# Optimization experiments

Measured on AMD Instinct MI355X. Metric: run time of the kernel, lower is better.

Reference implementation:

```python
import jax, jax.numpy as jnp
import numpy as np

VOCAB, EMBED, HIDDEN = 32000, 256, 1024
B, T = 64, 256


def setup_inputs() -> dict:
    key = jax.random.key(0)
    ks = jax.random.split(key, 8)
    s = 0.05
    return {
        "x": jax.random.randint(ks[0], (B, T), 0, VOCAB),
        "embed_table": jax.random.normal(ks[1], (VOCAB, EMBED), jnp.float32) * s,
        "W_ih": jax.random.normal(ks[2], (4 * HIDDEN, EMBED), jnp.float32) * s,
        "W_hh": jax.random.normal(ks[3], (4 * HIDDEN, HIDDEN), jnp.float32) * s,
        "b_ih": jax.random.normal(ks[4], (4 * HIDDEN,), jnp.float32) * s,
        "b_hh": jax.random.normal(ks[5], (4 * HIDDEN,), jnp.float32) * s,
        "fc_W": jax.random.normal(ks[6], (VOCAB, HIDDEN), jnp.float32) * s,
        "fc_b": jax.random.normal(ks[7], (VOCAB,), jnp.float32) * s,
    }


def _lstm_last_hidden(emb, W_ih, W_hh, b_ih, b_hh):
    # emb: [B, T, E]. PyTorch gate order: i, f, g, o.
    H = W_hh.shape[1]
    # Precompute input-side gate projections for all steps: [T, B, 4H]
    x_gates = jnp.einsum('bte,ge->tbg', emb, W_ih) + (b_ih + b_hh)

    def step(carry, xg):
        h, c = carry
        z = xg + h @ W_hh.T  # [B, 4H]
        i = jax.nn.sigmoid(z[:, 0 * H:1 * H])
        f = jax.nn.sigmoid(z[:, 1 * H:2 * H])
        g = jnp.tanh(z[:, 2 * H:3 * H])
        o = jax.nn.sigmoid(z[:, 3 * H:4 * H])
        c = f * c + i * g
        h = o * jnp.tanh(c)
        return (h, c), None

    bsz = emb.shape[0]
    h0 = jnp.zeros((bsz, H), emb.dtype)
    (h, _), _ = jax.lax.scan(step, (h0, h0), x_gates)
    return h  # last hidden state [B, H]


def reference(x, embed_table, W_ih, W_hh, b_ih, b_hh, fc_W, fc_b):
    emb = embed_table[x]  # [B, T, E]
    h_last = _lstm_last_hidden(emb, W_ih, W_hh, b_ih, b_hh)
    return h_last @ fc_W.T + fc_b  # [B, VOCAB]
```

## Files before the change

### kernel.cpp

```cpp
#include <hip/hip_runtime.h>
#include <hip/hip_bf16.h>

#define VOCAB  32000
#define EMBED  256
#define HIDDEN 1024
#define G4     4096
#define BATCH  64
#define SEQ    256

__global__ __launch_bounds__(256) void lstm_xgates(
    const int* __restrict__ x,
    const float* __restrict__ emb,
    const float* __restrict__ W_ih,
    const float* __restrict__ b_ih,
    const float* __restrict__ b_hh,
    float* __restrict__ xgT)
{
    const int t   = blockIdx.y;
    const int n0  = blockIdx.x * 64;
    const int tid = threadIdx.x;
    const int ty  = tid >> 4;
    const int tx  = tid & 15;

    __shared__ float As[64][36];
    __shared__ float Bs[64][36];
    __shared__ int   ridx[64];

    if (tid < 64) ridx[tid] = x[tid * SEQ + t];
    __syncthreads();

    float acc[4][4];
#pragma unroll
    for (int i = 0; i < 4; ++i)
#pragma unroll
        for (int j = 0; j < 4; ++j) acc[i][j] = 0.f;

    const int lr = tid >> 2;
    const int lc = (tid & 3) * 8;
    const float* abase = W_ih + (long)(n0 + lr) * EMBED + lc;
    const float* bbase = emb + (long)ridx[lr] * EMBED + lc;

    for (int k0 = 0; k0 < EMBED; k0 += 32) {
        *(float4*)&As[lr][lc]     = *(const float4*)(abase + k0);
        *(float4*)&As[lr][lc + 4] = *(const float4*)(abase + k0 + 4);
        *(float4*)&Bs[lr][lc]     = *(const float4*)(bbase + k0);
        *(float4*)&Bs[lr][lc + 4] = *(const float4*)(bbase + k0 + 4);
        __syncthreads();

#pragma unroll
        for (int kk = 0; kk < 32; kk += 4) {
            float4 av[4], bv[4];
#pragma unroll
            for (int i = 0; i < 4; ++i) av[i] = *(const float4*)&As[ty + 16 * i][kk];
#pragma unroll
            for (int j = 0; j < 4; ++j) bv[j] = *(const float4*)&Bs[tx + 16 * j][kk];
#pragma unroll
            for (int i = 0; i < 4; ++i)
#pragma unroll
                for (int j = 0; j < 4; ++j)
                    acc[i][j] += av[i].x * bv[j].x + av[i].y * bv[j].y
                               + av[i].z * bv[j].z + av[i].w * bv[j].w;
        }
        __syncthreads();
    }

#pragma unroll
    for (int i = 0; i < 4; ++i) {
        const int n = n0 + ty + 16 * i;
        const float bias = b_ih[n] + b_hh[n];
#pragma unroll
        for (int j = 0; j < 4; ++j) {
            const int b = tx + 16 * j;
            xgT[((long)t * G4 + n) * BATCH + b] = acc[i][j] + bias;
        }
    }
}

__global__ void lstm_init(float* __restrict__ h0, float* __restrict__ c)
{
    const int i = blockIdx.x * blockDim.x + threadIdx.x;
    if (i < BATCH * HIDDEN) { h0[i] = 0.f; c[i] = 0.f; }
}

__global__ __launch_bounds__(512, 1) void lstm_step(
    const float* __restrict__ W_hh,
    const float* __restrict__ xgT_t,
    const float* __restrict__ h_in,
    float* __restrict__ h_out,
    float* __restrict__ c)
{
    const int tile = blockIdx.x;
    const int tid  = threadIdx.x;
    const int w    = __builtin_amdgcn_readfirstlane(tid >> 6);
    const int b    = tid & 63;

    __shared__ float Wlds[16][1024];
    __shared__ float Zs[8][16][64];

    const float4* hin4 = (const float4*)h_in;
    const float4* W4   = (const float4*)W_hh;
    float4*       WL4  = (float4*)&Wlds[0][0];

    float4 wst[8];
#pragma unroll
    for (int i = 0; i < 8; ++i) {
        const int f     = tid + i * 512;
        const int row16 = f >> 8;
        const int k4i   = f & 255;
        const int grow  = ((row16 >> 2) << 10) + (tile << 2) + (row16 & 3);
        wst[i] = W4[(long)grow * 256 + k4i];
    }

    float xgv[4] = {0.f, 0.f, 0.f, 0.f};
    if (w < 4) {
#pragma unroll
        for (int g = 0; g < 4; ++g)
            xgv[g] = xgT_t[((long)(g << 10) + (tile << 2) + w) * BATCH + b];
    }

    float4 stc[4], stn[4];
#pragma unroll
    for (int i = 0; i < 4; ++i)
        stc[i] = hin4[(w * 32 + i) * 64 + b];

#pragma unroll
    for (int i = 0; i < 8; ++i) WL4[tid + i * 512] = wst[i];
    __syncthreads();

    float acc[16];
#pragma unroll
    for (int r = 0; r < 16; ++r) acc[r] = 0.f;

#pragma unroll
    for (int s = 0; s < 8; ++s) {
        if (s < 7) {
#pragma unroll
            for (int i = 0; i < 4; ++i)
                stn[i] = hin4[(w * 32 + (s + 1) * 4 + i) * 64 + b];
        }
#pragma unroll
        for (int kk = 0; kk < 4; ++kk) {
            const float4 h4 = stc[kk];
            const int    k4 = w * 32 + s * 4 + kk;
#pragma unroll
            for (int r = 0; r < 16; ++r) {
                const float4 wv = *(const float4*)&Wlds[r][k4 * 4];
                acc[r] = fmaf(wv.x, h4.x, acc[r]);
                acc[r] = fmaf(wv.y, h4.y, acc[r]);
                acc[r] = fmaf(wv.z, h4.z, acc[r]);
                acc[r] = fmaf(wv.w, h4.w, acc[r]);
            }
        }
#pragma unroll
        for (int i = 0; i < 4; ++i) stc[i] = stn[i];
    }

#pragma unroll
    for (int r = 0; r < 16; ++r) Zs[w][r][b] = acc[r];
    __syncthreads();

    if (w < 4) {
        const int jj = w;
        float z[4];
#pragma unroll
        for (int g = 0; g < 4; ++g) {
            float sum = xgv[g];
#pragma unroll
            for (int wp = 0; wp < 8; ++wp)
                sum += Zs[wp][g * 4 + jj][b];
            z[g] = sum;
        }
        const float ig = 1.f / (1.f + __expf(-z[0]));
        const float fg = 1.f / (1.f + __expf(-z[1]));
        const float gg = tanhf(z[2]);
        const float og = 1.f / (1.f + __expf(-z[3]));
        float* cp = c + (tile * 64 + b) * 4 + jj;
        const float cn = fg * (*cp) + ig * gg;
        *cp = cn;
        h_out[(tile * 64 + b) * 4 + jj] = og * tanhf(cn);
    }
}

__global__ __launch_bounds__(256) void lstm_fc(
    const float* __restrict__ h,
    const float* __restrict__ fc_W,
    const float* __restrict__ fc_b,
    float* __restrict__ out)
{
    const int v0  = blockIdx.x * 64;
    const int tid = threadIdx.x;
    const int ty  = tid >> 4;
    const int tx  = tid & 15;

    __shared__ float Hs[64][36];
    __shared__ float Ws[64][36];

    float acc[4][4];
#pragma unroll
    for (int i = 0; i < 4; ++i)
#pragma unroll
        for (int j = 0; j < 4; ++j) acc[i][j] = 0.f;

    const int lr = tid >> 2;
    const int lc = (tid & 3) * 8;
    const float4* h4 = (const float4*)h;
    const float* wbase = fc_W + (long)(v0 + lr) * HIDDEN + lc;

    for (int k0 = 0; k0 < HIDDEN; k0 += 32) {
        *(float4*)&Hs[lr][lc]     = h4[((k0 + lc) >> 2) * 64 + lr];
        *(float4*)&Hs[lr][lc + 4] = h4[((k0 + lc + 4) >> 2) * 64 + lr];
        *(float4*)&Ws[lr][lc]     = *(const float4*)(wbase + k0);
        *(float4*)&Ws[lr][lc + 4] = *(const float4*)(wbase + k0 + 4);
        __syncthreads();

#pragma unroll
        for (int kk = 0; kk < 32; kk += 4) {
            float4 hv[4], wv[4];
#pragma unroll
            for (int i = 0; i < 4; ++i) hv[i] = *(const float4*)&Hs[ty + 16 * i][kk];
#pragma unroll
            for (int j = 0; j < 4; ++j) wv[j] = *(const float4*)&Ws[tx + 16 * j][kk];
#pragma unroll
            for (int i = 0; i < 4; ++i)
#pragma unroll
                for (int j = 0; j < 4; ++j)
                    acc[i][j] += hv[i].x * wv[j].x + hv[i].y * wv[j].y
                               + hv[i].z * wv[j].z + hv[i].w * wv[j].w;
        }
        __syncthreads();
    }

#pragma unroll
    for (int j = 0; j < 4; ++j) {
        const int v = v0 + tx + 16 * j;
        const float bias = fc_b[v];
#pragma unroll
        for (int i = 0; i < 4; ++i) {
            const int b = ty + 16 * i;
            out[(long)b * VOCAB + v] = acc[i][j] + bias;
        }
    }
}

extern "C" void kernel_launch(void* const* d_in, const int* in_sizes, int n_in,
                              void* d_out, int out_size, void* d_ws, size_t ws_size,
                              hipStream_t stream)
{
    const int*   x     = (const int*)d_in[0];
    const float* emb   = (const float*)d_in[1];
    const float* W_ih  = (const float*)d_in[2];
    const float* W_hh  = (const float*)d_in[3];
    const float* b_ih  = (const float*)d_in[4];
    const float* b_hh  = (const float*)d_in[5];
    const float* fc_W  = (const float*)d_in[6];
    const float* fc_b  = (const float*)d_in[7];
    float* out = (float*)d_out;

    float* xgT = (float*)d_ws;
    float* hA  = xgT + (long)SEQ * G4 * BATCH;
    float* hB  = hA + BATCH * HIDDEN;
    float* c   = hB + BATCH * HIDDEN;

    lstm_xgates<<<dim3(G4 / 64, SEQ), 256, 0, stream>>>(x, emb, W_ih, b_ih, b_hh, xgT);
    lstm_init<<<dim3(BATCH * HIDDEN / 256), 256, 0, stream>>>(hA, c);

    float* hb[2] = {hA, hB};
    for (int t = 0; t < SEQ; ++t) {
        lstm_step<<<dim3(HIDDEN / 4), 512, 0, stream>>>(
            W_hh, xgT + (long)t * G4 * BATCH, hb[t & 1], hb[(t + 1) & 1], c);
    }
    lstm_fc<<<dim3(VOCAB / 64), 256, 0, stream>>>(hA, fc_W, fc_b, out);
}
```

Baseline: 4.205 ms.

## Use split-bf16 MFMA for LSTM recurrent matmul with pre-packed W_hh fragments

The recurrent h@W_hh^T per step now runs on MFMA 16x16x32 bf16 instructions instead of scalar FP32 FMAs from LDS. A one-time prep kernel splits W_hh into bf16 hi/lo parts laid out as MFMA B fragments, and each step loads them straight into registers, so the per-step LDS staging of the weight tile goes away. The hidden state is stored as hi/lo bf16 pairs and three MFMA products approximate FP32 accuracy. This adds a prep pass and some precision risk, and the FC kernel must rebuild h from the hi/lo pairs.

```diff
diff --git a/kernel.cpp b/kernel.cpp
--- a/kernel.cpp
+++ b/kernel.cpp
@@ -7,6 +7,46 @@
 #define G4     4096
 #define BATCH  64
 #define SEQ    256
+
+typedef short s16x8 __attribute__((ext_vector_type(8)));
+typedef float f32x4 __attribute__((ext_vector_type(4)));
+
+static __device__ __forceinline__ unsigned short f2bf(float f) {
+    unsigned u = __float_as_uint(f);
+    unsigned r = (u + 0x7fffu + ((u >> 16) & 1u)) >> 16;
+    return (unsigned short)r;
+}
+static __device__ __forceinline__ float bf2f(unsigned short s) {
+    return __uint_as_float(((unsigned)s) << 16);
+}
+
+__global__ __launch_bounds__(256) void lstm_wprep(
+    const float* __restrict__ W_hh,
+    unsigned short* __restrict__ Wf)
+{
+    const int tile = blockIdx.x;
+    const int ky   = blockIdx.y;
+    const int tid  = threadIdx.x;
+    const int wv   = tid >> 6;
+    const int lane = tid & 63;
+    const int ks   = ky * 4 + wv;
+    const int r    = lane & 15;
+    const int g    = lane >> 4;
+    const int grow = (r >> 2) * 1024 + tile * 4 + (r & 3);
+    const float* src = W_hh + (long)grow * 1024 + ks * 32 + g * 8;
+
+    s16x8 hi, lo;
+#pragma unroll
+    for (int e = 0; e < 8; ++e) {
+        const float v = src[e];
+        const unsigned short h = f2bf(v);
+        hi[e] = (short)h;
+        lo[e] = (short)f2bf(v - bf2f(h));
+    }
+    s16x8* dst = (s16x8*)(Wf + ((long)(tile * 32 + ks) * 2) * 512) + lane;
+    dst[0]  = hi;
+    dst[64] = lo;
+}
 
 __global__ __launch_bounds__(256) void lstm_xgates(
     const int* __restrict__ x,
@@ -76,113 +116,121 @@
     }
 }
 
-__global__ void lstm_init(float* __restrict__ h0, float* __restrict__ c)
+__global__ void lstm_init(float* __restrict__ c,
+                          unsigned short* __restrict__ hhi,
+                          unsigned short* __restrict__ hlo)
 {
     const int i = blockIdx.x * blockDim.x + threadIdx.x;
-    if (i < BATCH * HIDDEN) { h0[i] = 0.f; c[i] = 0.f; }
+    if (i < BATCH * HIDDEN) { c[i] = 0.f; hhi[i] = 0; hlo[i] = 0; }
 }
 
 __global__ __launch_bounds__(512, 1) void lstm_step(
-    const float* __restrict__ W_hh,
+    const unsigned short* __restrict__ Wf,
     const float* __restrict__ xgT_t,
-    const float* __restrict__ h_in,
-    float* __restrict__ h_out,
+    const unsigned short* __restrict__ hHi_in,
+    const unsigned short* __restrict__ hLo_in,
+    unsigned short* __restrict__ hHi_out,
+    unsigned short* __restrict__ hLo_out,
     float* __restrict__ c)
 {
     const int tile = blockIdx.x;
     const int tid  = threadIdx.x;
     const int w    = __builtin_amdgcn_readfirstlane(tid >> 6);
-    const int b    = tid & 63;
-
-    __shared__ float Wlds[16][1024];
-    __shared__ float Zs[8][16][64];
-
-    const float4* hin4 = (const float4*)h_in;
-    const float4* W4   = (const float4*)W_hh;
-    float4*       WL4  = (float4*)&Wlds[0][0];
-
-    float4 wst[8];
-#pragma unroll
-    for (int i = 0; i < 8; ++i) {
-        const int f     = tid + i * 512;
-        const int row16 = f >> 8;
-        const int k4i   = f & 255;
-        const int grow  = ((row16 >> 2) << 10) + (tile << 2) + (row16 & 3);
-        wst[i] = W4[(long)grow * 256 + k4i];
+    const int lane = tid & 63;
+    const int r16  = lane & 15;
+    const int g    = lane >> 4;
+
+    __shared__ float Zs[8 * 16 * 66];
+
+    const s16x8* Wf8 = (const s16x8*)Wf;
+    const s16x8* hh8 = (const s16x8*)hHi_in;
+    const s16x8* hl8 = (const s16x8*)hLo_in;
+
+    s16x8 Whi[4], Wlo[4];
+#pragma unroll
+    for (int s = 0; s < 4; ++s) {
+        const long bi = ((long)(tile * 32 + w * 4 + s) * 2) * 64 + lane;
+        Whi[s] = Wf8[bi];
+        Wlo[s] = Wf8[bi + 64];
     }
 
     float xgv[4] = {0.f, 0.f, 0.f, 0.f};
     if (w < 4) {
 #pragma unroll
-        for (int g = 0; g < 4; ++g)
-            xgv[g] = xgT_t[((long)(g << 10) + (tile << 2) + w) * BATCH + b];
-    }
-
-    float4 stc[4], stn[4];
-#pragma unroll
-    for (int i = 0; i < 4; ++i)
-        stc[i] = hin4[(w * 32 + i) * 64 + b];
-
-#pragma unroll
-    for (int i = 0; i < 8; ++i) WL4[tid + i * 512] = wst[i];
-    __syncthreads();
-
-    float acc[16];
-#pragma unroll
-    for (int r = 0; r < 16; ++r) acc[r] = 0.f;
-
-#pragma unroll
-    for (int s = 0; s < 8; ++s) {
-        if (s < 7) {
-#pragma unroll
-            for (int i = 0; i < 4; ++i)
-                stn[i] = hin4[(w * 32 + (s + 1) * 4 + i) * 64 + b];
-        }
-#pragma unroll
-        for (int kk = 0; kk < 4; ++kk) {
-            const float4 h4 = stc[kk];
-            const int    k4 = w * 32 + s * 4 + kk;
-#pragma unroll
-            for (int r = 0; r < 16; ++r) {
-                const float4 wv = *(const float4*)&Wlds[r][k4 * 4];
-                acc[r] = fmaf(wv.x, h4.x, acc[r]);
-                acc[r] = fmaf(wv.y, h4.y, acc[r]);
-                acc[r] = fmaf(wv.z, h4.z, acc[r]);
-                acc[r] = fmaf(wv.w, h4.w, acc[r]);
+        for (int gg = 0; gg < 4; ++gg)
+            xgv[gg] = xgT_t[((long)(gg << 10) + (tile << 2) + w) * BATCH + lane];
+    }
+
+    f32x4 acc[4];
+#pragma unroll
+    for (int m = 0; m < 4; ++m) acc[m] = (f32x4){0.f, 0.f, 0.f, 0.f};
+
+    s16x8 ah[2][4], al[2][4];
+#pragma unroll
+    for (int m = 0; m < 4; ++m) {
+        const int hidx = (m * 16 + r16) * 128 + (w * 4) * 4 + g;
+        ah[0][m] = hh8[hidx];
+        al[0][m] = hl8[hidx];
+    }
+
+#pragma unroll
+    for (int s = 0; s < 4; ++s) {
+        const int cur = s & 1, nxt = cur ^ 1;
+        if (s < 3) {
+#pragma unroll
+            for (int m = 0; m < 4; ++m) {
+                const int hidx = (m * 16 + r16) * 128 + (w * 4 + s + 1) * 4 + g;
+                ah[nxt][m] = hh8[hidx];
+                al[nxt][m] = hl8[hidx];
             }
         }
 #pragma unroll
-        for (int i = 0; i < 4; ++i) stc[i] = stn[i];
-    }
-
-#pragma unroll
-    for (int r = 0; r < 16; ++r) Zs[w][r][b] = acc[r];
+        for (int m = 0; m < 4; ++m) {
+            acc[m] = __builtin_amdgcn_mfma_f32_16x16x32_bf16(ah[cur][m], Whi[s], acc[m], 0, 0, 0);
+            acc[m] = __builtin_amdgcn_mfma_f32_16x16x32_bf16(al[cur][m], Whi[s], acc[m], 0, 0, 0);
+            acc[m] = __builtin_amdgcn_mfma_f32_16x16x32_bf16(ah[cur][m], Wlo[s], acc[m], 0, 0, 0);
+        }
+    }
+
+#pragma unroll
+    for (int m = 0; m < 4; ++m)
+#pragma unroll
+        for (int q = 0; q < 4; ++q) {
+            const int b = m * 16 + g * 4 + q;
+            Zs[(w * 16 + r16) * 66 + b] = acc[m][q];
+        }
     __syncthreads();
 
     if (w < 4) {
         const int jj = w;
+        const int b  = lane;
         float z[4];
 #pragma unroll
-        for (int g = 0; g < 4; ++g) {
-            float sum = xgv[g];
+        for (int gg = 0; gg < 4; ++gg) {
+            float sum = xgv[gg];
 #pragma unroll
             for (int wp = 0; wp < 8; ++wp)
-                sum += Zs[wp][g * 4 + jj][b];
-            z[g] = sum;
+                sum += Zs[(wp * 16 + gg * 4 + jj) * 66 + b];
+            z[gg] = sum;
         }
         const float ig = 1.f / (1.f + __expf(-z[0]));
         const float fg = 1.f / (1.f + __expf(-z[1]));
-        const float gg = tanhf(z[2]);
+        const float gt = tanhf(z[2]);
         const float og = 1.f / (1.f + __expf(-z[3]));
         float* cp = c + (tile * 64 + b) * 4 + jj;
-        const float cn = fg * (*cp) + ig * gg;
+        const float cn = fg * (*cp) + ig * gt;
         *cp = cn;
-        h_out[(tile * 64 + b) * 4 + jj] = og * tanhf(cn);
+        const float hn = og * tanhf(cn);
+        const unsigned short hhi = f2bf(hn);
+        const unsigned short hlo = f2bf(hn - bf2f(hhi));
+        hHi_out[b * HIDDEN + tile * 4 + jj] = hhi;
+        hLo_out[b * HIDDEN + tile * 4 + jj] = hlo;
     }
 }
 
 __global__ __launch_bounds__(256) void lstm_fc(
-    const float* __restrict__ h,
+    const unsigned short* __restrict__ h_hi,
+    const unsigned short* __restrict__ h_lo,
     const float* __restrict__ fc_W,
     const float* __restrict__ fc_b,
     float* __restrict__ out)
@@ -203,12 +251,17 @@
 
     const int lr = tid >> 2;
     const int lc = (tid & 3) * 8;
-    const float4* h4 = (const float4*)h;
+    const s16x8* hi8 = (const s16x8*)h_hi;
+    const s16x8* lo8 = (const s16x8*)h_lo;
     const float* wbase = fc_W + (long)(v0 + lr) * HIDDEN + lc;
 
     for (int k0 = 0; k0 < HIDDEN; k0 += 32) {
-        *(float4*)&Hs[lr][lc]     = h4[((k0 + lc) >> 2) * 64 + lr];
-        *(float4*)&Hs[lr][lc + 4] = h4[((k0 + lc + 4) >> 2) * 64 + lr];
+        const int hidx = lr * 128 + ((k0 + lc) >> 3);
+        const s16x8 vh = hi8[hidx];
+        const s16x8 vl = lo8[hidx];
+#pragma unroll
+        for (int e = 0; e < 8; ++e)
+            Hs[lr][lc + e] = bf2f((unsigned short)vh[e]) + bf2f((unsigned short)vl[e]);
         *(float4*)&Ws[lr][lc]     = *(const float4*)(wbase + k0);
         *(float4*)&Ws[lr][lc + 4] = *(const float4*)(wbase + k0 + 4);
         __syncthreads();
@@ -257,17 +310,23 @@
     float* out = (float*)d_out;
 
     float* xgT = (float*)d_ws;
-    float* hA  = xgT + (long)SEQ * G4 * BATCH;
-    float* hB  = hA + BATCH * HIDDEN;
-    float* c   = hB + BATCH * HIDDEN;
-
+    unsigned short* Wf   = (unsigned short*)(xgT + (long)SEQ * G4 * BATCH);
+    unsigned short* hHiA = Wf + (long)256 * 32 * 2 * 512;
+    unsigned short* hLoA = hHiA + BATCH * HIDDEN;
+    unsigned short* hHiB = hLoA + BATCH * HIDDEN;
+    unsigned short* hLoB = hHiB + BATCH * HIDDEN;
+    float* c = (float*)(hLoB + BATCH * HIDDEN);
+
+    lstm_wprep<<<dim3(256, 8), 256, 0, stream>>>(W_hh, Wf);
     lstm_xgates<<<dim3(G4 / 64, SEQ), 256, 0, stream>>>(x, emb, W_ih, b_ih, b_hh, xgT);
-    lstm_init<<<dim3(BATCH * HIDDEN / 256), 256, 0, stream>>>(hA, c);
-
-    float* hb[2] = {hA, hB};
+    lstm_init<<<dim3(BATCH * HIDDEN / 256), 256, 0, stream>>>(c, hHiA, hLoA);
+
+    unsigned short* hhi[2] = {hHiA, hHiB};
+    unsigned short* hlo[2] = {hLoA, hLoB};
     for (int t = 0; t < SEQ; ++t) {
         lstm_step<<<dim3(HIDDEN / 4), 512, 0, stream>>>(
-            W_hh, xgT + (long)t * G4 * BATCH, hb[t & 1], hb[(t + 1) & 1], c);
-    }
-    lstm_fc<<<dim3(VOCAB / 64), 256, 0, stream>>>(hA, fc_W, fc_b, out);
-}
+            Wf, xgT + (long)t * G4 * BATCH,
+            hhi[t & 1], hlo[t & 1], hhi[(t + 1) & 1], hlo[(t + 1) & 1], c);
+    }
+    lstm_fc<<<dim3(VOCAB / 64), 256, 0, stream>>>(hHiA, hLoA, fc_W, fc_b, out);
+}
```

Measured after the change: 4.006 ms. 4.7% less time.
